# Optimization experiments

Measured on AMD Instinct MI355X. Metric: run time of the kernel, lower is better.

The kernel has to match this reference:

```python
import jax, jax.numpy as jnp
import numpy as np

EPS = 1e-5
NHEAD = 8
NEG = -1e9  # matches -inf masked-fill semantics; rows never fully masked after fallback


def layer_norm(x, g, b):
    m = jnp.mean(x, axis=-1, keepdims=True)
    v = jnp.var(x, axis=-1, keepdims=True)
    return (x - m) * jax.lax.rsqrt(v + EPS) * g + b


def mha(q, k, v, Wqkv, bqkv, Wo, bo, bias=None):
    # torch nn.MultiheadAttention math (batch_first). Wqkv: [C, 3C] (jax layout).
    B, N, C = q.shape
    M = k.shape[1]
    d = C // NHEAD
    Wq, Wk, Wv = jnp.split(Wqkv, 3, axis=1)
    bq, bk, bv = jnp.split(bqkv, 3)
    qp = (q @ Wq + bq).reshape(B, N, NHEAD, d)
    kp = (k @ Wk + bk).reshape(B, M, NHEAD, d)
    vp = (v @ Wv + bv).reshape(B, M, NHEAD, d)
    s = jnp.einsum('bnhd,bmhd->bhnm', qp, kp) / np.sqrt(d).astype(q.dtype)
    if bias is not None:
        s = s + bias  # [B,1,N,M] broadcast over heads
    a = jax.nn.softmax(s, axis=-1)
    o = jnp.einsum('bhnm,bmhd->bnhd', a, vp).reshape(B, N, C)
    return o @ Wo + bo


def setup_inputs() -> dict:
    key = jax.random.key(0)
    B, Nq, HW, C, F = 8, 100, 4096, 512, 2048
    ks = jax.random.split(key, 16)
    s = 0.02
    inp = {
        'q': jax.random.normal(ks[0], (B, Nq, C), jnp.float32),
        'kv': jax.random.normal(ks[1], (B, HW, C), jnp.float32),
        'mask_bin': jax.random.randint(ks[2], (B, Nq, HW), 0, 2, jnp.int32),
        # MaskedXAttn: attn params + norm_q/norm_kv
        'xa_Wqkv': jax.random.normal(ks[3], (C, 3 * C), jnp.float32) * s,
        'xa_bqkv': jnp.zeros((3 * C,), jnp.float32),
        'xa_Wo': jax.random.normal(ks[4], (C, C), jnp.float32) * s,
        'xa_bo': jnp.zeros((C,), jnp.float32),
        'xa_gq': jnp.ones((C,), jnp.float32),
        'xa_bq_ln': jnp.zeros((C,), jnp.float32),
        'xa_gkv': jnp.ones((C,), jnp.float32),
        'xa_bkv_ln': jnp.zeros((C,), jnp.float32),
        # self-attention
        'sa_Wqkv': jax.random.normal(ks[5], (C, 3 * C), jnp.float32) * s,
        'sa_bqkv': jnp.zeros((3 * C,), jnp.float32),
        'sa_Wo': jax.random.normal(ks[6], (C, C), jnp.float32) * s,
        'sa_bo': jnp.zeros((C,), jnp.float32),
        # norms
        'n1_g': jnp.ones((C,), jnp.float32), 'n1_b': jnp.zeros((C,), jnp.float32),
        'n2_g': jnp.ones((C,), jnp.float32), 'n2_b': jnp.zeros((C,), jnp.float32),
        # FFN (MLP with num_layers=2: Linear(C,F), ReLU, Linear(F,C))
        'ff_W1': jax.random.normal(ks[7], (C, F), jnp.float32) * s,
        'ff_b1': jnp.zeros((F,), jnp.float32),
        'ff_W2': jax.random.normal(ks[8], (F, C), jnp.float32) * s,
        'ff_b2': jnp.zeros((C,), jnp.float32),
    }
    return inp


def reference(q, kv, mask_bin,
              xa_Wqkv, xa_bqkv, xa_Wo, xa_bo, xa_gq, xa_bq_ln, xa_gkv, xa_bkv_ln,
              sa_Wqkv, sa_bqkv, sa_Wo, sa_bo,
              n1_g, n1_b, n2_g, n2_b,
              ff_W1, ff_b1, ff_W2, ff_b2):
    # --- masked cross-attention (vectorized equivalent of per-query loop) ---
    qn = layer_norm(q, xa_gq, xa_bq_ln)
    kvn = layer_norm(kv, xa_gkv, xa_bkv_ln)
    allow = mask_bin.astype(bool)                      # [B,Nq,HW] True = attend
    row_any = jnp.any(allow, axis=-1, keepdims=True)   # queries with empty mask -> full attention
    eff = jnp.where(row_any, allow, True)
    bias = jnp.where(eff, 0.0, NEG).astype(q.dtype)[:, None, :, :]  # [B,1,Nq,HW]
    xa = mha(qn, kvn, kvn, xa_Wqkv, xa_bqkv, xa_Wo, xa_bo, bias=bias)
    q = q + xa
    # --- self-attention over queries ---
    qn1 = layer_norm(q, n1_g, n1_b)
    sa = mha(qn1, qn1, qn1, sa_Wqkv, sa_bqkv, sa_Wo, sa_bo)
    q = q + sa
    # --- FFN ---
    qn2 = layer_norm(q, n2_g, n2_b)
    h = jax.nn.relu(qn2 @ ff_W1 + ff_b1)
    q = q + (h @ ff_W2 + ff_b2)
    return q
```

## Files before the change

### kernel.cpp

```cpp
#include <hip/hip_runtime.h>

typedef unsigned short u16;
typedef unsigned int u32;
typedef __bf16 bf16x8 __attribute__((ext_vector_type(8)));
typedef short s16x4 __attribute__((ext_vector_type(4)));
typedef float f32x4 __attribute__((ext_vector_type(4)));

#define NEG_INF -3.0e38f
#define QSCALE 0.18033688011f

__device__ __forceinline__ u16 f2bf(float f){
  union { float f; u32 u; } v; v.f = f;
  u32 r = v.u + 0x7fffu + ((v.u >> 16) & 1u);
  return (u16)(r >> 16);
}
__device__ __forceinline__ float bf2f(u16 h){
  union { u32 u; float f; } v; v.u = ((u32)h) << 16; return v.f;
}
__device__ __forceinline__ short f2bf_s(float f){
  union { __bf16 h; short s; } cv; cv.h = (__bf16)f; return cv.s;
}

__device__ __forceinline__ f32x4 mfma16(s16x4 a, s16x4 b, f32x4 c){
#if __has_builtin(__builtin_amdgcn_mfma_f32_16x16x16bf16_1k)
  return __builtin_amdgcn_mfma_f32_16x16x16bf16_1k(a, b, c, 0, 0, 0);
#else
  asm("v_mfma_f32_16x16x16_bf16 %0, %1, %2, %0" : "+v"(c) : "v"(a), "v"(b));
  return c;
#endif
}

__device__ __forceinline__ void gl_lds16(const void* g, void* l){
  __builtin_amdgcn_global_load_lds((const __attribute__((address_space(1))) void*)g,
      (__attribute__((address_space(3))) void*)l, 16, 0, 0);
}

__device__ __forceinline__ void ln_body(const float* __restrict__ xr,
    const float* __restrict__ g, const float* __restrict__ b,
    u16* __restrict__ orow, int lane){
  float4 v0 = *(const float4*)(xr + lane * 4);
  float4 v1 = *(const float4*)(xr + 256 + lane * 4);
  float s = v0.x+v0.y+v0.z+v0.w + v1.x+v1.y+v1.z+v1.w;
  float q = v0.x*v0.x+v0.y*v0.y+v0.z*v0.z+v0.w*v0.w
          + v1.x*v1.x+v1.y*v1.y+v1.z*v1.z+v1.w*v1.w;
  #pragma unroll
  for (int d=1; d<64; d<<=1){ s += __shfl_xor(s, d, 64); q += __shfl_xor(q, d, 64); }
  float mean = s * (1.0f/512.0f);
  float var  = q * (1.0f/512.0f) - mean*mean;
  float rs = rsqrtf(var + 1e-5f);
  float4 g0 = *(const float4*)(g + lane*4), g1 = *(const float4*)(g + 256 + lane*4);
  float4 b0 = *(const float4*)(b + lane*4), b1 = *(const float4*)(b + 256 + lane*4);
  uint2 pa, pb;
  pa.x = (u32)f2bf((v0.x-mean)*rs*g0.x + b0.x) | ((u32)f2bf((v0.y-mean)*rs*g0.y + b0.y) << 16);
  pa.y = (u32)f2bf((v0.z-mean)*rs*g0.z + b0.z) | ((u32)f2bf((v0.w-mean)*rs*g0.w + b0.w) << 16);
  pb.x = (u32)f2bf((v1.x-mean)*rs*g1.x + b1.x) | ((u32)f2bf((v1.y-mean)*rs*g1.y + b1.y) << 16);
  pb.y = (u32)f2bf((v1.z-mean)*rs*g1.z + b1.z) | ((u32)f2bf((v1.w-mean)*rs*g1.w + b1.w) << 16);
  *(uint2*)(orow + lane*4) = pa;
  *(uint2*)(orow + 256 + lane*4) = pb;
}

__global__ __launch_bounds__(256) void ln_rows(const float* __restrict__ x,
    const float* __restrict__ g, const float* __restrict__ b,
    u16* __restrict__ out, int rows){
  int wid = threadIdx.x >> 6, lane = threadIdx.x & 63;
  int row = blockIdx.x * 4 + wid;
  if (row >= rows) return;
  ln_body(x + (size_t)row*512, g, b, out + (size_t)row*512, lane);
}

__global__ __launch_bounds__(256) void ln_all(
    const float* __restrict__ x0, const float* __restrict__ g0, const float* __restrict__ b0,
    u16* __restrict__ o0, int nb0, int rows0,
    const float* __restrict__ x1, const float* __restrict__ g1, const float* __restrict__ b1,
    u16* __restrict__ o1, int rows1){
  int wid = threadIdx.x >> 6, lane = threadIdx.x & 63;
  int bb = blockIdx.x;
  if (bb < nb0){
    int row = bb*4 + wid;
    if (row >= rows0) return;
    ln_body(x0 + (size_t)row*512, g0, b0, o0 + (size_t)row*512, lane);
  } else {
    int row = (bb - nb0)*4 + wid;
    if (row >= rows1) return;
    ln_body(x1 + (size_t)row*512, g1, b1, o1 + (size_t)row*512, lane);
  }
}

__global__ __launch_bounds__(128) void mask_prep(const int* __restrict__ mask, u32* __restrict__ mw){
  int r = blockIdx.x;
  int t = threadIdx.x;
  const int* mr = mask + (size_t)r*4096 + t*32;
  u32 w = 0;
  #pragma unroll
  for (int j=0;j<32;j+=4){
    int4 v = *(const int4*)(mr + j);
    w |= (u32)(v.x!=0) << j;
    w |= (u32)(v.y!=0) << (j+1);
    w |= (u32)(v.z!=0) << (j+2);
    w |= (u32)(v.w!=0) << (j+3);
  }
  int any = __syncthreads_or((int)(w != 0));
  mw[(size_t)r*128 + t] = any ? w : 0xffffffffu;
}

struct WtJobs {
  const float* W[7]; u16* Wt[7];
  int K[7], Nfull[7], ncol0[7], nt[7], blk0[7];
};

__global__ __launch_bounds__(256) void wtrans_all(WtJobs J){
  __shared__ float tile[32][33];
  const float* W = J.W[0]; u16* Wt = J.Wt[0];
  int K = J.K[0], Nfull = J.Nfull[0], ncol0 = J.ncol0[0], nt = J.nt[0], blk0 = 0;
  #pragma unroll
  for (int i=1;i<7;i++)
    if ((int)blockIdx.x >= J.blk0[i]){
      W=J.W[i]; Wt=J.Wt[i]; K=J.K[i]; Nfull=J.Nfull[i]; ncol0=J.ncol0[i]; nt=J.nt[i]; blk0=J.blk0[i];
    }
  int lb = blockIdx.x - blk0;
  int tk = lb / nt, tn = lb % nt;
  int t = threadIdx.x;
  int col = t & 31, kr = t >> 5;
  #pragma unroll
  for (int i=0;i<4;i++){
    int k = tk*32 + kr + i*8;
    tile[kr + i*8][col] = W[(size_t)k*Nfull + ncol0 + tn*32 + col];
  }
  __syncthreads();
  int nl = t >> 3, kc = (t & 7) * 4;
  uint2 o;
  o.x = (u32)f2bf(tile[kc+0][nl]) | ((u32)f2bf(tile[kc+1][nl]) << 16);
  o.y = (u32)f2bf(tile[kc+2][nl]) | ((u32)f2bf(tile[kc+3][nl]) << 16);
  *(uint2*)(Wt + (size_t)(tn*32 + nl)*K + tk*32 + kc) = o;
}

template<int EPI>
__global__ __launch_bounds__(256) void gemm_bt(
    const u16* __restrict__ A, const u16* __restrict__ Bt, const float* __restrict__ bias,
    float* __restrict__ outf, u16* __restrict__ outb, const float* __restrict__ res,
    int Mrows, int N, int K, int scale_cols,
    int T1, int rows_per_b, int vstride, u16* __restrict__ out2, int swz, int brmap)
{
  __shared__ __align__(16) u16 As[128*64];
  __shared__ __align__(16) u16 Bs[128*64];
  int bid = blockIdx.x;
  if (swz){ int cpx = gridDim.x >> 3; bid = (bid & 7)*cpx + (bid >> 3); }
  int NT = N >> 7;
  int mt = bid / NT, nt = bid % NT;
  int m0 = mt << 7, n0 = nt << 7;
  int tid = threadIdx.x;
  int wid = tid >> 6, lane = tid & 63;
  int wm = wid >> 1, wn = wid & 1;
  int lg = lane >> 4, l15 = lane & 15;

  f32x4 acc[4][4] = {};
  int ktiles = K >> 6;
  for (int kt = 0; kt < ktiles; ++kt){
    int k0 = kt << 6;
    if (kt) __syncthreads();
    #pragma unroll
    for (int i=0;i<4;i++){
      int L = i*4096 + tid*16;
      int T = L ^ (((L>>7)&7)<<4);
      int row = T >> 7, colb = T & 127;
      int ga = m0 + row; if (ga > Mrows-1) ga = Mrows-1;
      gl_lds16((const char*)A + ((size_t)ga*K + k0)*2 + colb, (char*)As + L);
    }
    #pragma unroll
    for (int i=0;i<4;i++){
      int L = i*4096 + tid*16;
      int T = L ^ (((L>>7)&7)<<4);
      int row = T >> 7, colb = T & 127;
      int rowg = n0 + row;
      if (brmap){ int rb = rowg & 127; rowg = (rowg>>7)*brmap + (rb < brmap ? rb : brmap-1); }
      gl_lds16((const char*)Bt + ((size_t)rowg*K + k0)*2 + colb, (char*)Bs + L);
    }
    __syncthreads();
    #pragma unroll
    for (int ks=0; ks<2; ++ks){
      bf16x8 af[4], bfr[4];
      #pragma unroll
      for (int mi=0; mi<4; ++mi){
        int r = wm*64 + mi*16 + l15;
        int byt = r*128 + ks*64 + lg*16;
        af[mi] = *(const bf16x8*)((const char*)As + (byt ^ ((r&7)<<4)));
      }
      #pragma unroll
      for (int ni=0; ni<4; ++ni){
        int r = wn*64 + ni*16 + l15;
        int byt = r*128 + ks*64 + lg*16;
        bfr[ni] = *(const bf16x8*)((const char*)Bs + (byt ^ ((r&7)<<4)));
      }
      __builtin_amdgcn_s_setprio(1);
      #pragma unroll
      for (int mi=0;mi<4;mi++)
        #pragma unroll
        for (int ni=0;ni<4;ni++)
          acc[mi][ni] = __builtin_amdgcn_mfma_f32_16x16x32_bf16(af[mi], bfr[ni], acc[mi][ni], 0,0,0);
      __builtin_amdgcn_s_setprio(0);
    }
  }

  if (EPI == 3){
    float bv[4];
    #pragma unroll
    for (int ni=0;ni<4;ni++) bv[ni] = bias[n0 + wn*64 + ni*16 + l15];
    #pragma unroll
    for (int ni=0;ni<4;ni++){
      int c = n0 + wn*64 + ni*16 + l15;
      #pragma unroll
      for (int mi=0;mi<4;mi++){
        int mr0 = m0 + wm*64 + mi*16 + lg*4;
        if (mr0 >= Mrows) continue;
        if (c < T1){
          #pragma unroll
          for (int r4=0;r4<4;r4++)
            outb[(size_t)(mr0+r4)*T1 + c] = f2bf(acc[mi][ni][r4] + bv[ni]);
        } else {
          int bidx = mr0 / rows_per_b;
          int key  = mr0 - bidx*rows_per_b;
          uint2 o;
          o.x = (u32)f2bf(acc[mi][ni][0]+bv[ni]) | ((u32)f2bf(acc[mi][ni][1]+bv[ni])<<16);
          o.y = (u32)f2bf(acc[mi][ni][2]+bv[ni]) | ((u32)f2bf(acc[mi][ni][3]+bv[ni])<<16);
          *(uint2*)(out2 + ((size_t)bidx*512 + (c - T1))*vstride + key) = o;
        }
      }
    }
  } else if (EPI == 4){
    #pragma unroll
    for (int mi=0;mi<4;mi++){
      #pragma unroll
      for (int r4=0;r4<4;r4++){
        int m = m0 + wm*64 + mi*16 + lg*4 + r4;
        if (m >= Mrows) continue;
        float rb = bias[m];
        #pragma unroll
        for (int ni=0;ni<4;ni++){
          int c = n0 + wn*64 + ni*16 + l15;
          outb[(size_t)m*N + c] = f2bf(acc[mi][ni][r4] + rb);
        }
      }
    }
  } else {
    float bv[4], scl[4];
    #pragma unroll
    for (int ni=0;ni<4;ni++){
      int c = n0 + wn*64 + ni*16 + l15;
      bv[ni]  = bias[c];
      scl[ni] = (c < scale_cols) ? QSCALE : 1.0f;
    }
    #pragma unroll
    for (int mi=0;mi<4;mi++){
      #pragma unroll
      for (int r4=0;r4<4;r4++){
        int m = m0 + wm*64 + mi*16 + lg*4 + r4;
        if (m >= Mrows) continue;
        #pragma unroll
        for (int ni=0;ni<4;ni++){
          int c = n0 + wn*64 + ni*16 + l15;
          float v = acc[mi][ni][r4] + bv[ni];
          if (EPI == 0){
            outb[(size_t)m*N + c] = f2bf(v*scl[ni]);
          } else if (EPI == 1){
            outb[(size_t)m*N + c] = f2bf(fmaxf(v, 0.0f));
          } else {
            outf[(size_t)m*N + c] = v + res[(size_t)m*N + c];
          }
        }
      }
    }
  }
}

template<bool PARTIAL, bool HASMASK, int NTILES>
__global__ __launch_bounds__(256) void attn_kernel(
    const u16* __restrict__ Qp, int ldq,
    const u16* __restrict__ Kp, int ldk, int kcol0,
    const u16* __restrict__ VT, size_t vbs, int vfs,
    const u32* __restrict__ maskw,
    float* __restrict__ pm, float* __restrict__ pl, u16* __restrict__ po,
    u16* __restrict__ o_out,
    int nq, int mk, int S, int H, int Bp, int swz)
{
  __shared__ __align__(16) u16 Ks[2*4096];
  __shared__ __align__(16) u16 Vs[2*4096];
  int bid = blockIdx.x;
  if (swz){ int cpx = gridDim.x >> 3; bid = (bid & 7)*cpx + (bid >> 3); }
  int s = bid % S; int h = (bid / S) % H; int b = bid / (S*H);
  int tid = threadIdx.x, wid = tid>>6, lane = tid&63;
  int lg = lane>>4, l15 = lane&15;
  int qbase = b*nq;
  int kps = mk / S;
  int kbeg = s * kps;
  int mwld = mk >> 5;
  int krel = lg*4;

  bf16x8 qf[2][2];
  #pragma unroll
  for (int mt=0;mt<2;mt++){
    int qr = wid*32 + mt*16 + l15; int qc = qr < nq ? qr : nq-1;
    #pragma unroll
    for (int ks=0;ks<2;ks++)
      qf[mt][ks] = *(const bf16x8*)(Qp + (size_t)(qbase+qc)*ldq + h*64 + ks*32 + lg*8);
  }
  u32 wmw[2][2*NTILES];
  if (HASMASK){
    #pragma unroll
    for (int mt=0;mt<2;mt++){
      int qr = wid*32 + mt*16 + lg*4;
      int qc = (wid*32 + mt*16 + l15) < nq ? (wid*32 + mt*16 + l15) : nq-1;
      const u32* mrow = maskw + (size_t)(qbase+qc)*mwld + (kbeg>>5);
      #pragma unroll
      for (int wi=0; wi<2*NTILES; wi+=4){
        uint4 v = *(const uint4*)(mrow + wi);
        wmw[mt][wi+0]=v.x; wmw[mt][wi+1]=v.y; wmw[mt][wi+2]=v.z; wmw[mt][wi+3]=v.w;
      }
      (void)qr;
    }
  }

  float m_r[2] = {NEG_INF, NEG_INF};
  float l_r[2] = {0.0f, 0.0f};
  f32x4 of[2][4] = {};

  auto stage = [&](int t_, int bufi){
    int kb_ = kbeg + t_*64;
    #pragma unroll
    for (int i=0;i<2;i++){
      int idx = i*256 + tid;
      int key = idx>>3, sd = idx&7;
      int kc = kb_ + key; if (kc > mk-1) kc = mk-1;
      const char* src = (const char*)(Kp + (size_t)(b*mk + kc)*ldk + kcol0 + h*64) + ((sd ^ (key&7))<<4);
      gl_lds16(src, (char*)Ks + bufi*8192 + idx*16);
    }
    #pragma unroll
    for (int i=0;i<2;i++){
      int idx = i*256 + tid;
      int f = idx>>3, sd = idx&7;
      const char* src = (const char*)(VT + (size_t)b*vbs + (size_t)(h*64+f)*vfs + kb_) + ((sd ^ (f&7))<<4);
      gl_lds16(src, (char*)Vs + bufi*8192 + idx*16);
    }
  };

  stage(0, 0);

  #pragma unroll
  for (int t=0;t<NTILES;t++){
    if (t+1 < NTILES){
      stage(t+1, (t+1)&1);
      asm volatile("s_waitcnt vmcnt(4)" ::: "memory");
    } else {
      asm volatile("s_waitcnt vmcnt(0)" ::: "memory");
    }
    __builtin_amdgcn_s_barrier();

    const char* Kb = (const char*)Ks + (t&1)*8192;
    const char* Vb = (const char*)Vs + (t&1)*8192;
    int kb = kbeg + t*64;

    f32x4 sT[4][2] = {};
    #pragma unroll
    for (int nt2=0;nt2<4;nt2++){
      bf16x8 k0 = *(const bf16x8*)(Kb + ((nt2*16+l15)<<7) + (((lg  ) ^ (l15&7))<<4));
      bf16x8 k1 = *(const bf16x8*)(Kb + ((nt2*16+l15)<<7) + (((4+lg) ^ (l15&7))<<4));
      __builtin_amdgcn_s_setprio(1);
      #pragma unroll
      for (int mt=0;mt<2;mt++){
        sT[nt2][mt] = __builtin_amdgcn_mfma_f32_16x16x32_bf16(k0, qf[mt][0], sT[nt2][mt], 0,0,0);
        sT[nt2][mt] = __builtin_amdgcn_mfma_f32_16x16x32_bf16(k1, qf[mt][1], sT[nt2][mt], 0,0,0);
      }
      __builtin_amdgcn_s_setprio(0);
    }

    s16x4 pb[2][4];
    #pragma unroll
    for (int mt=0;mt<2;mt++){
      float mx = NEG_INF;
      #pragma unroll
      for (int nt2=0;nt2<4;nt2++){
        u32 wb = 0;
        if (HASMASK) wb = wmw[mt][t*2 + (nt2>>1)] >> (((nt2&1)<<4) + krel);
        #pragma unroll
        for (int r=0;r<4;r++){
          bool ok = HASMASK ? (((wb>>r)&1u) != 0) : (kb + nt2*16 + krel + r < mk);
          float sv = ok ? sT[nt2][mt][r] : NEG_INF;
          sT[nt2][mt][r] = sv;
          mx = fmaxf(mx, sv);
        }
      }
      mx = fmaxf(mx, __shfl_xor(mx, 16, 64));
      mx = fmaxf(mx, __shfl_xor(mx, 32, 64));
      if (!__all(mx <= m_r[mt] + 8.0f)){
        float mnew = fmaxf(m_r[mt], mx);
        float corr = exp2f(m_r[mt] - mnew);
        m_r[mt] = mnew;
        l_r[mt] *= corr;
        #pragma unroll
        for (int nf=0;nf<4;nf++) of[mt][nf] *= corr;
      }
      float ps = 0.0f;
      #pragma unroll
      for (int nt2=0;nt2<4;nt2++)
        #pragma unroll
        for (int r=0;r<4;r++){
          float p = exp2f(sT[nt2][mt][r] - m_r[mt]);
          ps += p;
          pb[mt][nt2][r] = f2bf_s(p);
        }
      ps += __shfl_xor(ps, 16, 64);
      ps += __shfl_xor(ps, 32, 64);
      l_r[mt] += ps;
    }

    #pragma unroll
    for (int nf=0;nf<4;nf++){
      s16x4 vf[4];
      #pragma unroll
      for (int nt2=0;nt2<4;nt2++){
        int slot = (nt2*2 + (lg>>1)) ^ (l15&7);
        vf[nt2] = *(const s16x4*)(Vb + ((nf*16+l15)<<7) + (slot<<4) + ((lg&1)<<3));
      }
      __builtin_amdgcn_s_setprio(1);
      #pragma unroll
      for (int mt=0;mt<2;mt++)
        #pragma unroll
        for (int nt2=0;nt2<4;nt2++)
          of[mt][nf] = mfma16(vf[nt2], pb[mt][nt2], of[mt][nf]);
      __builtin_amdgcn_s_setprio(0);
    }
    __builtin_amdgcn_s_barrier();
  }

  #pragma unroll
  for (int mt=0;mt<2;mt++){
    int q = wid*32 + mt*16 + l15;
    if (q < nq){
      if (PARTIAL){
        size_t base = (((size_t)(s*Bp + b)*H + h)*128 + q);
        if (lg == 0){ pm[base] = m_r[mt]; pl[base] = l_r[mt]; }
        #pragma unroll
        for (int nf=0;nf<4;nf++){
          uint2 o;
          o.x = (u32)f2bf(of[mt][nf][0]) | ((u32)f2bf(of[mt][nf][1])<<16);
          o.y = (u32)f2bf(of[mt][nf][2]) | ((u32)f2bf(of[mt][nf][3])<<16);
          *(uint2*)(po + base*64 + nf*16 + lg*4) = o;
        }
      } else {
        float inv = 1.0f / l_r[mt];
        #pragma unroll
        for (int nf=0;nf<4;nf++){
          uint2 o;
          o.x = (u32)f2bf(of[mt][nf][0]*inv) | ((u32)f2bf(of[mt][nf][1]*inv)<<16);
          o.y = (u32)f2bf(of[mt][nf][2]*inv) | ((u32)f2bf(of[mt][nf][3]*inv)<<16);
          *(uint2*)(o_out + (size_t)(qbase+q)*512 + h*64 + nf*16 + lg*4) = o;
        }
      }
    }
  }
}

__global__ __launch_bounds__(64) void attn_combine(
    const float* __restrict__ pm, const float* __restrict__ pl, const u16* __restrict__ po,
    u16* __restrict__ o_out, int S, int Bp, int H, int nq)
{
  int bid = blockIdx.x;
  int q = bid % nq; int h = (bid / nq) % H; int b = bid / (nq*H);
  int f = threadIdx.x;
  float mstar = NEG_INF;
  for (int s=0;s<S;s++){
    size_t idx = (((size_t)(s*Bp + b)*H + h)*128 + q);
    mstar = fmaxf(mstar, pm[idx]);
  }
  float L = 0.0f, acc = 0.0f;
  for (int s=0;s<S;s++){
    size_t idx = (((size_t)(s*Bp + b)*H + h)*128 + q);
    float w = exp2f(pm[idx] - mstar);
    L += w * pl[idx];
    acc += w * bf2f(po[idx*64 + f]);
  }
  o_out[((size_t)b*nq + q)*512 + h*64 + f] = f2bf(acc / L);
}

extern "C" void kernel_launch(void* const* d_in, const int* in_sizes, int n_in,
                              void* d_out, int out_size, void* d_ws, size_t ws_size,
                              hipStream_t stream){
  const float* q_in    = (const float*)d_in[0];
  const float* kv_in   = (const float*)d_in[1];
  const int*   maskb   = (const int*)d_in[2];
  const float* xa_Wqkv = (const float*)d_in[3];
  const float* xa_bqkv = (const float*)d_in[4];
  const float* xa_Wo   = (const float*)d_in[5];
  const float* xa_bo   = (const float*)d_in[6];
  const float* xa_gq   = (const float*)d_in[7];
  const float* xa_bq   = (const float*)d_in[8];
  const float* xa_gkv  = (const float*)d_in[9];
  const float* xa_bkv  = (const float*)d_in[10];
  const float* sa_Wqkv = (const float*)d_in[11];
  const float* sa_bqkv = (const float*)d_in[12];
  const float* sa_Wo   = (const float*)d_in[13];
  const float* sa_bo   = (const float*)d_in[14];
  const float* n1_g = (const float*)d_in[15];
  const float* n1_b = (const float*)d_in[16];
  const float* n2_g = (const float*)d_in[17];
  const float* n2_b = (const float*)d_in[18];
  const float* ff_W1 = (const float*)d_in[19];
  const float* ff_b1 = (const float*)d_in[20];
  const float* ff_W2 = (const float*)d_in[21];
  const float* ff_b2 = (const float*)d_in[22];

  char* ws = (char*)d_ws;
  size_t off = 0;
  auto alloc = [&](size_t bytes)->char*{ char* p = ws + off; off = (off + bytes + 255) & ~(size_t)255; return p; };
  u16* wq  = (u16*)alloc((size_t)512*512*2);
  u16* wkv = (u16*)alloc((size_t)1024*512*2);
  u16* wsa = (u16*)alloc((size_t)1536*512*2);
  u16* wxo = (u16*)alloc((size_t)512*512*2);
  u16* wso = (u16*)alloc((size_t)512*512*2);
  u16* wf1 = (u16*)alloc((size_t)2048*512*2);
  u16* wf2 = (u16*)alloc((size_t)512*2048*2);
  u16* qn  = (u16*)alloc((size_t)800*512*2);
  u16* qp  = (u16*)alloc((size_t)800*512*2);
  u32* mw  = (u32*)alloc((size_t)800*128*4);
  u16* kp  = (u16*)alloc((size_t)32768*512*2);
  u16* vpT = (u16*)alloc((size_t)8*512*4096*2);
  size_t reuse_off = off;
  u16* kvn = (u16*)alloc((size_t)32768*512*2);
  size_t offB = reuse_off;
  auto allocB = [&](size_t bytes)->char*{ char* p = ws + offB; offB = (offB + bytes + 255) & ~(size_t)255; return p; };
  const int S = 16;
  float* pm   = (float*)allocB((size_t)S*64*128*4);
  float* pl   = (float*)allocB((size_t)S*64*128*4);
  u16*   po   = (u16*)allocB((size_t)S*64*128*64*2);
  u16* o_xa   = (u16*)allocB((size_t)800*512*2);
  float* x1   = (float*)allocB((size_t)800*512*4);
  u16* qn1    = (u16*)allocB((size_t)800*512*2);
  u16* saqkv  = (u16*)allocB((size_t)800*1024*2);
  u16* vT2sa  = (u16*)allocB((size_t)512*1024*2);
  u16* o_sa   = (u16*)allocB((size_t)800*512*2);
  float* x2   = (float*)allocB((size_t)800*512*4);
  u16* qn2    = (u16*)allocB((size_t)800*512*2);
  u16* hbuf   = (u16*)allocB((size_t)800*2048*2);

  WtJobs J;
  J.W[0]=xa_Wqkv; J.Wt[0]=wq;  J.K[0]=512;  J.Nfull[0]=1536; J.ncol0[0]=0;   J.nt[0]=16;
  J.W[1]=xa_Wqkv; J.Wt[1]=wkv; J.K[1]=512;  J.Nfull[1]=1536; J.ncol0[1]=512; J.nt[1]=32;
  J.W[2]=sa_Wqkv; J.Wt[2]=wsa; J.K[2]=512;  J.Nfull[2]=1536; J.ncol0[2]=0;   J.nt[2]=48;
  J.W[3]=xa_Wo;   J.Wt[3]=wxo; J.K[3]=512;  J.Nfull[3]=512;  J.ncol0[3]=0;   J.nt[3]=16;
  J.W[4]=sa_Wo;   J.Wt[4]=wso; J.K[4]=512;  J.Nfull[4]=512;  J.ncol0[4]=0;   J.nt[4]=16;
  J.W[5]=ff_W1;   J.Wt[5]=wf1; J.K[5]=512;  J.Nfull[5]=2048; J.ncol0[5]=0;   J.nt[5]=64;
  J.W[6]=ff_W2;   J.Wt[6]=wf2; J.K[6]=2048; J.Nfull[6]=512;  J.ncol0[6]=0;   J.nt[6]=16;
  int tot = 0;
  for (int i=0;i<7;i++){ J.blk0[i] = tot; tot += (J.K[i]/32)*J.nt[i]; }
  wtrans_all<<<tot, 256, 0, stream>>>(J);

  ln_all<<<200+8192, 256, 0, stream>>>(q_in, xa_gq, xa_bq, qn, 200, 800,
                                       kv_in, xa_gkv, xa_bkv, kvn, 32768);
  mask_prep<<<800, 128, 0, stream>>>(maskb, mw);

  gemm_bt<0><<<7*4, 256, 0, stream>>>(qn, wq, xa_bqkv, nullptr, qp, nullptr,
                                      800, 512, 512, 512, 0, 1, 1, nullptr, 0, 0);
  gemm_bt<3><<<256*8, 256, 0, stream>>>(kvn, wkv, xa_bqkv+512, nullptr, kp, nullptr,
                                        32768, 1024, 512, 0, 512, 4096, 4096, vpT, 1, 0);
  attn_kernel<true,true,4><<<8*8*S, 256, 0, stream>>>(
      qp, 512, kp, 512, 0, vpT, (size_t)512*4096, 4096, mw,
      pm, pl, po, nullptr, 100, 4096, S, 8, 8, 1);
  attn_combine<<<8*8*100, 64, 0, stream>>>(pm, pl, po, o_xa, S, 8, 8, 100);
  gemm_bt<2><<<7*4, 256, 0, stream>>>(o_xa, wxo, xa_bo, x1, nullptr, q_in,
                                      800, 512, 512, 0, 0, 1, 1, nullptr, 0, 0);
  ln_rows<<<200, 256, 0, stream>>>(x1, n1_g, n1_b, qn1, 800);
  gemm_bt<0><<<7*8, 256, 0, stream>>>(qn1, wsa, sa_bqkv, nullptr, saqkv, nullptr,
                                      800, 1024, 512, 512, 0, 1, 1, nullptr, 0, 0);
  gemm_bt<4><<<4*8, 256, 0, stream>>>(wsa + (size_t)1024*512, qn1, sa_bqkv+1024,
                                      nullptr, vT2sa, nullptr,
                                      512, 1024, 512, 0, 0, 1, 1, nullptr, 0, 100);
  attn_kernel<false,false,2><<<64, 256, 0, stream>>>(
      saqkv, 1024, saqkv, 1024, 512, vT2sa, (size_t)128, 1024, nullptr,
      nullptr, nullptr, nullptr, o_sa, 100, 100, 1, 8, 8, 0);
  gemm_bt<2><<<7*4, 256, 0, stream>>>(o_sa, wso, sa_bo, x2, nullptr, x1,
                                      800, 512, 512, 0, 0, 1, 1, nullptr, 0, 0);
  ln_rows<<<200, 256, 0, stream>>>(x2, n2_g, n2_b, qn2, 800);
  gemm_bt<1><<<7*16, 256, 0, stream>>>(qn2, wf1, ff_b1, nullptr, hbuf, nullptr,
                                       800, 2048, 512, 0, 0, 1, 1, nullptr, 0, 0);
  gemm_bt<2><<<7*4, 256, 0, stream>>>(hbuf, wf2, ff_b2, (float*)d_out, nullptr, x2,
                                      800, 512, 2048, 0, 0, 1, 1, nullptr, 0, 0);
}
```

Measured before the change: 254.0 us.

## Double-buffer GEMM loads, batch independent GEMMs per launch, fold mask prep into LN

```diff
diff --git a/kernel.cpp b/kernel.cpp
--- a/kernel.cpp
+++ b/kernel.cpp
@@ -72,35 +72,39 @@
     const float* __restrict__ x0, const float* __restrict__ g0, const float* __restrict__ b0,
     u16* __restrict__ o0, int nb0, int rows0,
     const float* __restrict__ x1, const float* __restrict__ g1, const float* __restrict__ b1,
-    u16* __restrict__ o1, int rows1){
-  int wid = threadIdx.x >> 6, lane = threadIdx.x & 63;
+    u16* __restrict__ o1, int nb1, int rows1,
+    const int* __restrict__ mask, u32* __restrict__ mw){
+  __shared__ unsigned long long blds[4];
+  int tid = threadIdx.x;
+  int wid = tid >> 6, lane = tid & 63;
   int bb = blockIdx.x;
   if (bb < nb0){
     int row = bb*4 + wid;
     if (row >= rows0) return;
     ln_body(x0 + (size_t)row*512, g0, b0, o0 + (size_t)row*512, lane);
-  } else {
+  } else if (bb < nb0 + nb1){
     int row = (bb - nb0)*4 + wid;
     if (row >= rows1) return;
     ln_body(x1 + (size_t)row*512, g1, b1, o1 + (size_t)row*512, lane);
-  }
-}
-
-__global__ __launch_bounds__(128) void mask_prep(const int* __restrict__ mask, u32* __restrict__ mw){
-  int r = blockIdx.x;
-  int t = threadIdx.x;
-  const int* mr = mask + (size_t)r*4096 + t*32;
-  u32 w = 0;
-  #pragma unroll
-  for (int j=0;j<32;j+=4){
-    int4 v = *(const int4*)(mr + j);
-    w |= (u32)(v.x!=0) << j;
-    w |= (u32)(v.y!=0) << (j+1);
-    w |= (u32)(v.z!=0) << (j+2);
-    w |= (u32)(v.w!=0) << (j+3);
-  }
-  int any = __syncthreads_or((int)(w != 0));
-  mw[(size_t)r*128 + t] = any ? w : 0xffffffffu;
+  } else {
+    int lb = bb - nb0 - nb1;
+    int r0 = lb*2 + (wid >> 1);
+    int word = tid & 127;
+    const int* mr = mask + (size_t)r0*4096 + word*32;
+    u32 w = 0;
+    #pragma unroll
+    for (int j=0;j<32;j+=4){
+      int4 v = *(const int4*)(mr + j);
+      w |= (u32)(v.x!=0) << j;
+      w |= (u32)(v.y!=0) << (j+1);
+      w |= (u32)(v.z!=0) << (j+2);
+      w |= (u32)(v.w!=0) << (j+3);
+    }
+    blds[wid] = __ballot(w != 0);
+    __syncthreads();
+    bool any = (wid < 2) ? ((blds[0] | blds[1]) != 0ull) : ((blds[2] | blds[3]) != 0ull);
+    mw[(size_t)r0*128 + word] = any ? w : 0xffffffffu;
+  }
 }
 
 struct WtJobs {
@@ -134,18 +138,21 @@
   *(uint2*)(Wt + (size_t)(tn*32 + nl)*K + tk*32 + kc) = o;
 }
 
-template<int EPI>
-__global__ __launch_bounds__(256) void gemm_bt(
-    const u16* __restrict__ A, const u16* __restrict__ Bt, const float* __restrict__ bias,
-    float* __restrict__ outf, u16* __restrict__ outb, const float* __restrict__ res,
-    int Mrows, int N, int K, int scale_cols,
-    int T1, int rows_per_b, int vstride, u16* __restrict__ out2, int swz, int brmap)
-{
-  __shared__ __align__(16) u16 As[128*64];
-  __shared__ __align__(16) u16 Bs[128*64];
-  int bid = blockIdx.x;
-  if (swz){ int cpx = gridDim.x >> 3; bid = (bid & 7)*cpx + (bid >> 3); }
-  int NT = N >> 7;
+struct GemmJob {
+  const u16* A; const u16* Bt; const float* bias;
+  float* outf; u16* outb; const float* res; u16* out2;
+  int M, N, K, scale_cols, T1, rows_per_b, vstride, swz, brmap, epi, blk0, nblk;
+};
+struct GemmJobs { GemmJob j[2]; int njobs; };
+
+__global__ __launch_bounds__(256) void gemm_multi(GemmJobs G){
+  __shared__ __align__(16) u16 As[2][8192];
+  __shared__ __align__(16) u16 Bs[2][8192];
+  GemmJob J = G.j[0];
+  if (G.njobs > 1 && (int)blockIdx.x >= G.j[1].blk0) J = G.j[1];
+  int bid = (int)blockIdx.x - J.blk0;
+  if (J.swz){ int cpx = J.nblk >> 3; bid = (bid & 7)*cpx + (bid >> 3); }
+  int NT = J.N >> 7;
   int mt = bid / NT, nt = bid % NT;
   int m0 = mt << 7, n0 = nt << 7;
   int tid = threadIdx.x;
@@ -153,18 +160,15 @@
   int wm = wid >> 1, wn = wid & 1;
   int lg = lane >> 4, l15 = lane & 15;
 
-  f32x4 acc[4][4] = {};
-  int ktiles = K >> 6;
-  for (int kt = 0; kt < ktiles; ++kt){
+  auto stage = [&](int kt, int bufi){
     int k0 = kt << 6;
-    if (kt) __syncthreads();
     #pragma unroll
     for (int i=0;i<4;i++){
       int L = i*4096 + tid*16;
       int T = L ^ (((L>>7)&7)<<4);
       int row = T >> 7, colb = T & 127;
-      int ga = m0 + row; if (ga > Mrows-1) ga = Mrows-1;
-      gl_lds16((const char*)A + ((size_t)ga*K + k0)*2 + colb, (char*)As + L);
+      int ga = m0 + row; if (ga > J.M-1) ga = J.M-1;
+      gl_lds16((const char*)J.A + ((size_t)ga*J.K + k0)*2 + colb, (char*)As[bufi] + L);
     }
     #pragma unroll
     for (int i=0;i<4;i++){
@@ -172,10 +176,24 @@
       int T = L ^ (((L>>7)&7)<<4);
       int row = T >> 7, colb = T & 127;
       int rowg = n0 + row;
-      if (brmap){ int rb = rowg & 127; rowg = (rowg>>7)*brmap + (rb < brmap ? rb : brmap-1); }
-      gl_lds16((const char*)Bt + ((size_t)rowg*K + k0)*2 + colb, (char*)Bs + L);
-    }
-    __syncthreads();
+      if (J.brmap){ int rb = rowg & 127; rowg = (rowg>>7)*J.brmap + (rb < J.brmap ? rb : J.brmap-1); }
+      gl_lds16((const char*)J.Bt + ((size_t)rowg*J.K + k0)*2 + colb, (char*)Bs[bufi] + L);
+    }
+  };
+
+  f32x4 acc[4][4] = {};
+  int ktiles = J.K >> 6;
+  stage(0, 0);
+  for (int kt = 0; kt < ktiles; ++kt){
+    if (kt+1 < ktiles){
+      stage(kt+1, (kt+1)&1);
+      asm volatile("s_waitcnt vmcnt(8)" ::: "memory");
+    } else {
+      asm volatile("s_waitcnt vmcnt(0)" ::: "memory");
+    }
+    __builtin_amdgcn_s_barrier();
+    const char* Ab = (const char*)As[kt&1];
+    const char* Bb = (const char*)Bs[kt&1];
     #pragma unroll
     for (int ks=0; ks<2; ++ks){
       bf16x8 af[4], bfr[4];
@@ -183,13 +201,13 @@
       for (int mi=0; mi<4; ++mi){
         int r = wm*64 + mi*16 + l15;
         int byt = r*128 + ks*64 + lg*16;
-        af[mi] = *(const bf16x8*)((const char*)As + (byt ^ ((r&7)<<4)));
+        af[mi] = *(const bf16x8*)(Ab + (byt ^ ((r&7)<<4)));
       }
       #pragma unroll
       for (int ni=0; ni<4; ++ni){
         int r = wn*64 + ni*16 + l15;
         int byt = r*128 + ks*64 + lg*16;
-        bfr[ni] = *(const bf16x8*)((const char*)Bs + (byt ^ ((r&7)<<4)));
+        bfr[ni] = *(const bf16x8*)(Bb + (byt ^ ((r&7)<<4)));
       }
       __builtin_amdgcn_s_setprio(1);
       #pragma unroll
@@ -199,45 +217,46 @@
           acc[mi][ni] = __builtin_amdgcn_mfma_f32_16x16x32_bf16(af[mi], bfr[ni], acc[mi][ni], 0,0,0);
       __builtin_amdgcn_s_setprio(0);
     }
-  }
-
-  if (EPI == 3){
+    __builtin_amdgcn_s_barrier();
+  }
+
+  if (J.epi == 3){
     float bv[4];
     #pragma unroll
-    for (int ni=0;ni<4;ni++) bv[ni] = bias[n0 + wn*64 + ni*16 + l15];
+    for (int ni=0;ni<4;ni++) bv[ni] = J.bias[n0 + wn*64 + ni*16 + l15];
     #pragma unroll
     for (int ni=0;ni<4;ni++){
       int c = n0 + wn*64 + ni*16 + l15;
       #pragma unroll
       for (int mi=0;mi<4;mi++){
         int mr0 = m0 + wm*64 + mi*16 + lg*4;
-        if (mr0 >= Mrows) continue;
-        if (c < T1){
+        if (mr0 >= J.M) continue;
+        if (c < J.T1){
           #pragma unroll
           for (int r4=0;r4<4;r4++)
-            outb[(size_t)(mr0+r4)*T1 + c] = f2bf(acc[mi][ni][r4] + bv[ni]);
+            J.outb[(size_t)(mr0+r4)*J.T1 + c] = f2bf(acc[mi][ni][r4] + bv[ni]);
         } else {
-          int bidx = mr0 / rows_per_b;
-          int key  = mr0 - bidx*rows_per_b;
+          int bidx = mr0 / J.rows_per_b;
+          int key  = mr0 - bidx*J.rows_per_b;
           uint2 o;
           o.x = (u32)f2bf(acc[mi][ni][0]+bv[ni]) | ((u32)f2bf(acc[mi][ni][1]+bv[ni])<<16);
           o.y = (u32)f2bf(acc[mi][ni][2]+bv[ni]) | ((u32)f2bf(acc[mi][ni][3]+bv[ni])<<16);
-          *(uint2*)(out2 + ((size_t)bidx*512 + (c - T1))*vstride + key) = o;
+          *(uint2*)(J.out2 + ((size_t)bidx*512 + (c - J.T1))*J.vstride + key) = o;
         }
       }
     }
-  } else if (EPI == 4){
+  } else if (J.epi == 4){
     #pragma unroll
     for (int mi=0;mi<4;mi++){
       #pragma unroll
       for (int r4=0;r4<4;r4++){
         int m = m0 + wm*64 + mi*16 + lg*4 + r4;
-        if (m >= Mrows) continue;
-        float rb = bias[m];
+        if (m >= J.M) continue;
+        float rb = J.bias[m];
         #pragma unroll
         for (int ni=0;ni<4;ni++){
           int c = n0 + wn*64 + ni*16 + l15;
-          outb[(size_t)m*N + c] = f2bf(acc[mi][ni][r4] + rb);
+          J.outb[(size_t)m*J.N + c] = f2bf(acc[mi][ni][r4] + rb);
         }
       }
     }
@@ -246,25 +265,25 @@
     #pragma unroll
     for (int ni=0;ni<4;ni++){
       int c = n0 + wn*64 + ni*16 + l15;
-      bv[ni]  = bias[c];
-      scl[ni] = (c < scale_cols) ? QSCALE : 1.0f;
+      bv[ni]  = J.bias[c];
+      scl[ni] = (c < J.scale_cols) ? QSCALE : 1.0f;
     }
     #pragma unroll
     for (int mi=0;mi<4;mi++){
       #pragma unroll
       for (int r4=0;r4<4;r4++){
         int m = m0 + wm*64 + mi*16 + lg*4 + r4;
-        if (m >= Mrows) continue;
+        if (m >= J.M) continue;
         #pragma unroll
         for (int ni=0;ni<4;ni++){
           int c = n0 + wn*64 + ni*16 + l15;
           float v = acc[mi][ni][r4] + bv[ni];
-          if (EPI == 0){
-            outb[(size_t)m*N + c] = f2bf(v*scl[ni]);
-          } else if (EPI == 1){
-            outb[(size_t)m*N + c] = f2bf(fmaxf(v, 0.0f));
+          if (J.epi == 0){
+            J.outb[(size_t)m*J.N + c] = f2bf(v*scl[ni]);
+          } else if (J.epi == 1){
+            J.outb[(size_t)m*J.N + c] = f2bf(fmaxf(v, 0.0f));
           } else {
-            outf[(size_t)m*N + c] = v + res[(size_t)m*N + c];
+            J.outf[(size_t)m*J.N + c] = v + J.res[(size_t)m*J.N + c];
           }
         }
       }
@@ -307,7 +326,6 @@
   if (HASMASK){
     #pragma unroll
     for (int mt=0;mt<2;mt++){
-      int qr = wid*32 + mt*16 + lg*4;
       int qc = (wid*32 + mt*16 + l15) < nq ? (wid*32 + mt*16 + l15) : nq-1;
       const u32* mrow = maskw + (size_t)(qbase+qc)*mwld + (kbeg>>5);
       #pragma unroll
@@ -315,7 +333,6 @@
         uint4 v = *(const uint4*)(mrow + wi);
         wmw[mt][wi+0]=v.x; wmw[mt][wi+1]=v.y; wmw[mt][wi+2]=v.z; wmw[mt][wi+3]=v.w;
       }
-      (void)qr;
     }
   }
 
@@ -553,34 +570,51 @@
   for (int i=0;i<7;i++){ J.blk0[i] = tot; tot += (J.K[i]/32)*J.nt[i]; }
   wtrans_all<<<tot, 256, 0, stream>>>(J);
 
-  ln_all<<<200+8192, 256, 0, stream>>>(q_in, xa_gq, xa_bq, qn, 200, 800,
-                                       kv_in, xa_gkv, xa_bkv, kvn, 32768);
-  mask_prep<<<800, 128, 0, stream>>>(maskb, mw);
-
-  gemm_bt<0><<<7*4, 256, 0, stream>>>(qn, wq, xa_bqkv, nullptr, qp, nullptr,
-                                      800, 512, 512, 512, 0, 1, 1, nullptr, 0, 0);
-  gemm_bt<3><<<256*8, 256, 0, stream>>>(kvn, wkv, xa_bqkv+512, nullptr, kp, nullptr,
-                                        32768, 1024, 512, 0, 512, 4096, 4096, vpT, 1, 0);
+  ln_all<<<200+8192+400, 256, 0, stream>>>(q_in, xa_gq, xa_bq, qn, 200, 800,
+                                           kv_in, xa_gkv, xa_bkv, kvn, 8192, 32768,
+                                           maskb, mw);
+
+  auto mkjob = [&](const u16*A, const u16*Bt, const float*bias, float*outf, u16*outb,
+                   const float*res, u16*out2, int M, int N, int K, int sc, int T1,
+                   int rpb, int vst, int swz, int brm, int epi, int blk0, int nblk)->GemmJob{
+    GemmJob j; j.A=A; j.Bt=Bt; j.bias=bias; j.outf=outf; j.outb=outb; j.res=res; j.out2=out2;
+    j.M=M; j.N=N; j.K=K; j.scale_cols=sc; j.T1=T1; j.rows_per_b=rpb; j.vstride=vst;
+    j.swz=swz; j.brmap=brm; j.epi=epi; j.blk0=blk0; j.nblk=nblk; return j;
+  };
+  auto run1 = [&](GemmJob a, int grid){
+    GemmJobs g; g.j[0]=a; g.j[1]=a; g.njobs=1;
+    gemm_multi<<<grid, 256, 0, stream>>>(g);
+  };
+  auto run2 = [&](GemmJob a, GemmJob b, int grid){
+    GemmJobs g; g.j[0]=a; g.j[1]=b; g.njobs=2;
+    gemm_multi<<<grid, 256, 0, stream>>>(g);
+  };
+
+  run2(mkjob(qn, wq, xa_bqkv, nullptr, qp, nullptr, nullptr,
+             800, 512, 512, 512, 0,1,1, 0,0, 0, 0, 28),
+       mkjob(kvn, wkv, xa_bqkv+512, nullptr, kp, nullptr, vpT,
+             32768, 1024, 512, 0, 512, 4096, 4096, 1, 0, 3, 28, 2048),
+       28 + 2048);
   attn_kernel<true,true,4><<<8*8*S, 256, 0, stream>>>(
       qp, 512, kp, 512, 0, vpT, (size_t)512*4096, 4096, mw,
       pm, pl, po, nullptr, 100, 4096, S, 8, 8, 1);
   attn_combine<<<8*8*100, 64, 0, stream>>>(pm, pl, po, o_xa, S, 8, 8, 100);
-  gemm_bt<2><<<7*4, 256, 0, stream>>>(o_xa, wxo, xa_bo, x1, nullptr, q_in,
-                                      800, 512, 512, 0, 0, 1, 1, nullptr, 0, 0);
+  run1(mkjob(o_xa, wxo, xa_bo, x1, nullptr, q_in, nullptr,
+             800, 512, 512, 0, 0,1,1, 0,0, 2, 0, 28), 28);
   ln_rows<<<200, 256, 0, stream>>>(x1, n1_g, n1_b, qn1, 800);
-  gemm_bt<0><<<7*8, 256, 0, stream>>>(qn1, wsa, sa_bqkv, nullptr, saqkv, nullptr,
-                                      800, 1024, 512, 512, 0, 1, 1, nullptr, 0, 0);
-  gemm_bt<4><<<4*8, 256, 0, stream>>>(wsa + (size_t)1024*512, qn1, sa_bqkv+1024,
-                                      nullptr, vT2sa, nullptr,
-                                      512, 1024, 512, 0, 0, 1, 1, nullptr, 0, 100);
+  run2(mkjob(qn1, wsa, sa_bqkv, nullptr, saqkv, nullptr, nullptr,
+             800, 1024, 512, 512, 0,1,1, 0,0, 0, 0, 56),
+       mkjob(wsa + (size_t)1024*512, qn1, sa_bqkv+1024, nullptr, vT2sa, nullptr, nullptr,
+             512, 1024, 512, 0, 0,1,1, 0, 100, 4, 56, 32),
+       56 + 32);
   attn_kernel<false,false,2><<<64, 256, 0, stream>>>(
       saqkv, 1024, saqkv, 1024, 512, vT2sa, (size_t)128, 1024, nullptr,
       nullptr, nullptr, nullptr, o_sa, 100, 100, 1, 8, 8, 0);
-  gemm_bt<2><<<7*4, 256, 0, stream>>>(o_sa, wso, sa_bo, x2, nullptr, x1,
-                                      800, 512, 512, 0, 0, 1, 1, nullptr, 0, 0);
+  run1(mkjob(o_sa, wso, sa_bo, x2, nullptr, x1, nullptr,
+             800, 512, 512, 0, 0,1,1, 0,0, 2, 0, 28), 28);
   ln_rows<<<200, 256, 0, stream>>>(x2, n2_g, n2_b, qn2, 800);
-  gemm_bt<1><<<7*16, 256, 0, stream>>>(qn2, wf1, ff_b1, nullptr, hbuf, nullptr,
-                                       800, 2048, 512, 0, 0, 1, 1, nullptr, 0, 0);
-  gemm_bt<2><<<7*4, 256, 0, stream>>>(hbuf, wf2, ff_b2, (float*)d_out, nullptr, x2,
-                                      800, 512, 2048, 0, 0, 1, 1, nullptr, 0, 0);
-}
+  run1(mkjob(qn2, wf1, ff_b1, nullptr, hbuf, nullptr, nullptr,
+             800, 2048, 512, 0, 0,1,1, 0,0, 1, 0, 112), 112);
+  run1(mkjob(hbuf, wf2, ff_b2, (float*)d_out, nullptr, x2, nullptr,
+             800, 512, 2048, 0, 0,1,1, 0,0, 2, 0, 28), 28);
+}
```

Result: slower. 285.6 us (+12.4%).
